# Kernel tuning notes

Hardware: AMD Instinct MI355X
Metric: run time of the kernel (lower is better)

The kernel has to match this reference:

```python
import jax, jax.numpy as jnp
import numpy as np

K = 5        # kernel_size per pseudo-dim
DIM = 2      # pseudo-coordinate dimensionality
K2 = K * K   # total kernel weight matrices
N_NODES = 50000


def spline_basis(edge_attr):
    """Open B-spline basis, degree=1, dim=2. Returns basis [E,4], weight_index [E,4]."""
    v = edge_attr * (K - 1)                      # [E,2], pseudo in [0,1]
    lo = jnp.floor(v)
    frac = v - lo                                # [E,2]
    lo = lo.astype(jnp.int32)
    fac = jnp.stack([1.0 - frac, frac], axis=-1)                 # [E,2,2] (dim, bit)
    idx = jnp.clip(lo[..., None] + jnp.arange(2), 0, K - 1)      # [E,2,2]
    b0 = jnp.array([0, 1, 0, 1])  # bit for dim 0, per spline term
    b1 = jnp.array([0, 0, 1, 1])  # bit for dim 1
    basis = fac[:, 0, b0] * fac[:, 1, b1]        # [E,4]
    wi = idx[:, 0, b0] * K + idx[:, 1, b1]       # [E,4] flat kernel index
    return basis, wi


def spline_conv(x, src, dst, basis, wi, W, root, bias, n_nodes):
    """SplineConv with mean aggregation, root weight and bias.
    x:[N,Fin] W:[K2,Fin,Fout] root:[Fin,Fout] bias:[Fout]"""
    E = src.shape[0]
    K2_, Fin, Fout = W.shape
    # scatter the 4 sparse basis values into a dense per-edge kernel-coeff matrix [E,K2]
    coeff = jnp.zeros((E, K2_), x.dtype).at[jnp.arange(E)[:, None], wi].add(basis)
    xj = x[src]                                  # gather source features [E,Fin]
    msg = jnp.zeros((E, Fout), x.dtype)
    for k in range(K2_):                         # fixed small loop over 25 kernels
        msg = msg + coeff[:, k:k + 1] * (xj @ W[k])
    agg = jax.ops.segment_sum(msg, dst, num_segments=n_nodes)    # [N,Fout]
    deg = jax.ops.segment_sum(jnp.ones((E,), x.dtype), dst, num_segments=n_nodes)
    agg = agg / jnp.clip(deg, 1.0)[:, None]      # mean aggregation
    return agg + x @ root + bias


def setup_inputs() -> dict:
    key = jax.random.key(0)
    ks = jax.random.split(key, 9)
    E = 800000
    Fin, H, C = 64, 16, 7
    x = jax.random.normal(ks[0], (N_NODES, Fin), dtype=jnp.float32)
    edge_index = jax.random.randint(ks[1], (2, E), 0, N_NODES, dtype=jnp.int64)
    edge_attr = jax.random.uniform(ks[2], (E, DIM), dtype=jnp.float32)
    s1 = 1.0 / np.sqrt(Fin)
    s2 = 1.0 / np.sqrt(H)
    W1 = jax.random.uniform(ks[3], (K2, Fin, H), jnp.float32, -s1, s1)
    root1 = jax.random.uniform(ks[4], (Fin, H), jnp.float32, -s1, s1)
    bias1 = jax.random.uniform(ks[5], (H,), jnp.float32, -s1, s1)
    W2 = jax.random.uniform(ks[6], (K2, H, C), jnp.float32, -s2, s2)
    root2 = jax.random.uniform(ks[7], (H, C), jnp.float32, -s2, s2)
    bias2 = jax.random.uniform(ks[8], (C,), jnp.float32, -s2, s2)
    return {"x": x, "edge_index": edge_index, "edge_attr": edge_attr,
            "W1": W1, "root1": root1, "bias1": bias1,
            "W2": W2, "root2": root2, "bias2": bias2}


def reference(x, edge_index, edge_attr, W1, root1, bias1, W2, root2, bias2):
    src = edge_index[0]
    dst = edge_index[1]
    basis, wi = spline_basis(edge_attr)
    h = jax.nn.relu(spline_conv(x, src, dst, basis, wi, W1, root1, bias1, N_NODES))
    # dropout(p=0.6) is identity in eval mode
    out = spline_conv(h, src, dst, basis, wi, W2, root2, bias2, N_NODES)
    return jax.nn.log_softmax(out, axis=1)
```

## Files before the change

kernel.cpp:

```cpp
#include <hip/hip_runtime.h>

#define KK2 25
#define FIN 64
#define HH 16
#define CC 7

#define SCAN_VPT 4
#define SCAN_BLK 256
#define SCAN_CHUNK (SCAN_VPT * SCAN_BLK)

__global__ void k_hist(const int* __restrict__ ei, int* __restrict__ cnt, int E) {
    int e = blockIdx.x * 256 + threadIdx.x;
    if (e < E) atomicAdd(&cnt[ei[E + e]], 1);
}

__global__ void k_bsum(const int* __restrict__ cnt, int* __restrict__ bsum, int N) {
    int b = blockIdx.x, t = threadIdx.x;
    int base = b * SCAN_CHUNK + t * SCAN_VPT;
    int s = 0;
#pragma unroll
    for (int j = 0; j < SCAN_VPT; j++) {
        int i = base + j;
        if (i < N) s += cnt[i];
    }
#pragma unroll
    for (int d = 1; d < 64; d <<= 1) s += __shfl_xor(s, d, 64);
    __shared__ int sd[SCAN_BLK / 64];
    if ((t & 63) == 0) sd[t >> 6] = s;
    __syncthreads();
    if (t == 0) {
        int tot = 0;
        for (int w = 0; w < SCAN_BLK / 64; w++) tot += sd[w];
        bsum[b] = tot;
    }
}

__global__ void k_bscan(const int* __restrict__ bsum, int* __restrict__ boff, int nblk) {
    int t = threadIdx.x;
    __shared__ int sd[256];
    int v = (t < nblk) ? bsum[t] : 0;
    sd[t] = v;
    __syncthreads();
    for (int off = 1; off < 256; off <<= 1) {
        int u = (t >= off) ? sd[t - off] : 0;
        __syncthreads();
        sd[t] += u;
        __syncthreads();
    }
    boff[t] = sd[t] - v;
}

__global__ void k_sfin(const int* __restrict__ cnt, const int* __restrict__ boff,
                       int* __restrict__ rowStart, int* __restrict__ cursor, int N) {
    int b = blockIdx.x, t = threadIdx.x;
    int base = b * SCAN_CHUNK + t * SCAN_VPT;
    int v[SCAN_VPT];
    int s = 0;
#pragma unroll
    for (int j = 0; j < SCAN_VPT; j++) {
        int i = base + j;
        v[j] = (i < N) ? cnt[i] : 0;
        s += v[j];
    }
    __shared__ int sd[SCAN_BLK];
    sd[t] = s;
    __syncthreads();
    for (int off = 1; off < SCAN_BLK; off <<= 1) {
        int u = (t >= off) ? sd[t - off] : 0;
        __syncthreads();
        sd[t] += u;
        __syncthreads();
    }
    int run = sd[t] - s + boff[b];
#pragma unroll
    for (int j = 0; j < SCAN_VPT; j++) {
        int i = base + j;
        if (i < N) {
            rowStart[i] = run;
            cursor[i] = run;
            run += v[j];
            if (i == N - 1) rowStart[N] = run;
        }
    }
}

__global__ void k_scatter(const float* __restrict__ attr, const int* __restrict__ ei,
                          int* __restrict__ cursor, int* __restrict__ eSrc,
                          float4* __restrict__ eBasis, unsigned* __restrict__ eWi, int E) {
    int e = blockIdx.x * 256 + threadIdx.x;
    if (e >= E) return;
    float v0 = attr[2 * e] * 4.0f, v1 = attr[2 * e + 1] * 4.0f;
    float l0 = floorf(v0), l1 = floorf(v1);
    float f0 = v0 - l0, f1 = v1 - l1;
    int i0 = (int)l0, i1 = (int)l1;
    int i0a = min(max(i0, 0), 4), i0b = min(max(i0 + 1, 0), 4);
    int i1a = min(max(i1, 0), 4), i1b = min(max(i1 + 1, 0), 4);
    float4 b;
    b.x = (1.0f - f0) * (1.0f - f1);
    b.y = f0 * (1.0f - f1);
    b.z = (1.0f - f0) * f1;
    b.w = f0 * f1;
    unsigned pack = (unsigned)(i0a * 5 + i1a) | ((unsigned)(i0b * 5 + i1a) << 8) |
                    ((unsigned)(i0a * 5 + i1b) << 16) | ((unsigned)(i0b * 5 + i1b) << 24);
    int s = ei[e], d = ei[E + e];
    int pos = atomicAdd(&cursor[d], 1);
    eSrc[pos] = s;
    eBasis[pos] = b;
    eWi[pos] = pack;
}

__global__ void k_prepW(const float* __restrict__ W1, const float* __restrict__ W2,
                        float* __restrict__ B1t, float* __restrict__ W2p) {
    int tid = blockIdx.x * 256 + threadIdx.x;
    if (tid < KK2 * FIN * HH) {
        int c = tid >> 6, i = tid & 63;
        int k = c >> 4, h = c & 15;
        B1t[tid] = W1[(k * FIN + i) * HH + h];
    }
    if (tid < KK2 * HH * CC) {
        int k = tid / (HH * CC), r = tid % (HH * CC);
        int i = r / CC, c = r % CC;
        W2p[(k * HH + i) * 8 + c] = W2[tid];
    }
}

__global__ void k_y1(const float* __restrict__ x, const float* __restrict__ B1t,
                     float* __restrict__ y1, int N, int nb) {
    int q = blockIdx.x / nb;
    int n = (blockIdx.x % nb) * 256 + threadIdx.x;
    if (n >= N) return;
    float4 xr[16];
    const float4* xp = (const float4*)(x + (size_t)n * 64);
#pragma unroll
    for (int i = 0; i < 16; i++) xr[i] = xp[i];
    const float* B = B1t + q * 100 * 64;
    float4* yo = (float4*)(y1 + (size_t)n * 400 + q * 100);
    for (int cg = 0; cg < 25; cg++) {
        float a0 = 0, a1 = 0, a2 = 0, a3 = 0;
        const float4* b0 = (const float4*)(B + (cg * 4 + 0) * 64);
        const float4* b1 = (const float4*)(B + (cg * 4 + 1) * 64);
        const float4* b2 = (const float4*)(B + (cg * 4 + 2) * 64);
        const float4* b3 = (const float4*)(B + (cg * 4 + 3) * 64);
#pragma unroll
        for (int i = 0; i < 16; i++) {
            float4 xi = xr[i];
            float4 v0 = b0[i], v1 = b1[i], v2 = b2[i], v3 = b3[i];
            a0 += xi.x * v0.x + xi.y * v0.y + xi.z * v0.z + xi.w * v0.w;
            a1 += xi.x * v1.x + xi.y * v1.y + xi.z * v1.z + xi.w * v1.w;
            a2 += xi.x * v2.x + xi.y * v2.y + xi.z * v2.z + xi.w * v2.w;
            a3 += xi.x * v3.x + xi.y * v3.y + xi.z * v3.z + xi.w * v3.w;
        }
        yo[cg] = make_float4(a0, a1, a2, a3);
    }
}

__global__ void k_agg1(const int* __restrict__ rowStart, const int* __restrict__ eSrc,
                       const float4* __restrict__ eBasis, const unsigned* __restrict__ eWi,
                       const float* __restrict__ y1, float* __restrict__ agg1, int N) {
    int n = blockIdx.x * 4 + (threadIdx.x >> 6);
    if (n >= N) return;
    int lane = threadIdx.x & 63;
    int sub = lane >> 4, h = lane & 15;
    int start = rowStart[n], end = rowStart[n + 1];
    float acc = 0.0f;
    for (int i = start + sub; i < end; i += 4) {
        int s = eSrc[i];
        float4 b = eBasis[i];
        unsigned w = eWi[i];
        const float* yr = y1 + (size_t)s * 400;
        acc += b.x * yr[(w & 255u) * 16 + h];
        acc += b.y * yr[((w >> 8) & 255u) * 16 + h];
        acc += b.z * yr[((w >> 16) & 255u) * 16 + h];
        acc += b.w * yr[(w >> 24) * 16 + h];
    }
    acc += __shfl_xor(acc, 16, 64);
    acc += __shfl_xor(acc, 32, 64);
    if (lane < 16) agg1[(size_t)n * 16 + h] = acc;
}

__global__ void k_upd1(const float* __restrict__ x, const float* __restrict__ agg1,
                       const int* __restrict__ rowStart, const float* __restrict__ root1,
                       const float* __restrict__ bias1, float* __restrict__ h1, int N) {
    int n = blockIdx.x * 256 + threadIdx.x;
    if (n >= N) return;
    float inv = 1.0f / (float)max(rowStart[n + 1] - rowStart[n], 1);
    float r[16];
#pragma unroll
    for (int h = 0; h < 16; h++) r[h] = agg1[(size_t)n * 16 + h] * inv + bias1[h];
    const float* xrow = x + (size_t)n * 64;
    for (int i = 0; i < 64; i++) {
        float xi = xrow[i];
        const float* rr = root1 + i * 16;
#pragma unroll
        for (int h = 0; h < 16; h++) r[h] += xi * rr[h];
    }
    float* ho = h1 + (size_t)n * 16;
#pragma unroll
    for (int h = 0; h < 16; h++) ho[h] = fmaxf(r[h], 0.0f);
}

__global__ void k_y2(const float* __restrict__ h1, const float* __restrict__ W2p,
                     float* __restrict__ y2, int N) {
    int n = blockIdx.x * 256 + threadIdx.x;
    if (n >= N) return;
    float h[16];
    const float4* hp = (const float4*)(h1 + (size_t)n * 16);
#pragma unroll
    for (int j = 0; j < 4; j++) {
        float4 v = hp[j];
        h[4 * j] = v.x; h[4 * j + 1] = v.y; h[4 * j + 2] = v.z; h[4 * j + 3] = v.w;
    }
    float4* yo = (float4*)(y2 + (size_t)n * 200);
    for (int k = 0; k < 25; k++) {
        float4 zlo = make_float4(0, 0, 0, 0), zhi = make_float4(0, 0, 0, 0);
        const float4* wp = (const float4*)(W2p + k * 128);
#pragma unroll
        for (int i = 0; i < 16; i++) {
            float hi = h[i];
            float4 lo = wp[2 * i], hv = wp[2 * i + 1];
            zlo.x += hi * lo.x; zlo.y += hi * lo.y; zlo.z += hi * lo.z; zlo.w += hi * lo.w;
            zhi.x += hi * hv.x; zhi.y += hi * hv.y; zhi.z += hi * hv.z; zhi.w += hi * hv.w;
        }
        yo[2 * k] = zlo;
        yo[2 * k + 1] = zhi;
    }
}

__global__ void k_agg2(const int* __restrict__ rowStart, const int* __restrict__ eSrc,
                       const float4* __restrict__ eBasis, const unsigned* __restrict__ eWi,
                       const float* __restrict__ y2, float* __restrict__ agg2, int N) {
    int n = blockIdx.x * 4 + (threadIdx.x >> 6);
    if (n >= N) return;
    int lane = threadIdx.x & 63;
    int sub = lane >> 3, c = lane & 7;
    int start = rowStart[n], end = rowStart[n + 1];
    float acc = 0.0f;
    for (int i = start + sub; i < end; i += 8) {
        int s = eSrc[i];
        float4 b = eBasis[i];
        unsigned w = eWi[i];
        const float* yr = y2 + (size_t)s * 200;
        acc += b.x * yr[(w & 255u) * 8 + c];
        acc += b.y * yr[((w >> 8) & 255u) * 8 + c];
        acc += b.z * yr[((w >> 16) & 255u) * 8 + c];
        acc += b.w * yr[(w >> 24) * 8 + c];
    }
    acc += __shfl_xor(acc, 8, 64);
    acc += __shfl_xor(acc, 16, 64);
    acc += __shfl_xor(acc, 32, 64);
    if (lane < 8) agg2[(size_t)n * 8 + c] = acc;
}

__global__ void k_fin2(const float* __restrict__ h1, const float* __restrict__ agg2,
                       const int* __restrict__ rowStart, const float* __restrict__ root2,
                       const float* __restrict__ bias2, float* __restrict__ out, int N) {
    int n = blockIdx.x * 256 + threadIdx.x;
    if (n >= N) return;
    float inv = 1.0f / (float)max(rowStart[n + 1] - rowStart[n], 1);
    float z[7];
#pragma unroll
    for (int c = 0; c < 7; c++) z[c] = agg2[(size_t)n * 8 + c] * inv + bias2[c];
    const float* hrow = h1 + (size_t)n * 16;
#pragma unroll
    for (int i = 0; i < 16; i++) {
        float hi = hrow[i];
        const float* rr = root2 + i * 7;
#pragma unroll
        for (int c = 0; c < 7; c++) z[c] += hi * rr[c];
    }
    float m = z[0];
#pragma unroll
    for (int c = 1; c < 7; c++) m = fmaxf(m, z[c]);
    float ssum = 0.0f;
#pragma unroll
    for (int c = 0; c < 7; c++) ssum += expf(z[c] - m);
    float ls = logf(ssum);
    float* orow = out + (size_t)n * 7;
#pragma unroll
    for (int c = 0; c < 7; c++) orow[c] = z[c] - m - ls;
}

extern "C" void kernel_launch(void* const* d_in, const int* in_sizes, int n_in,
                              void* d_out, int out_size, void* d_ws, size_t ws_size,
                              hipStream_t stream) {
    const float* x     = (const float*)d_in[0];
    const int*   ei    = (const int*)d_in[1];
    const float* attr  = (const float*)d_in[2];
    const float* W1    = (const float*)d_in[3];
    const float* root1 = (const float*)d_in[4];
    const float* bias1 = (const float*)d_in[5];
    const float* W2    = (const float*)d_in[6];
    const float* root2 = (const float*)d_in[7];
    const float* bias2 = (const float*)d_in[8];
    float* out = (float*)d_out;

    int N = in_sizes[0] / FIN;
    int E = in_sizes[1] / 2;

    char* w = (char*)d_ws;
    size_t off = 0;
    auto alloc = [&](size_t bytes) -> void* {
        void* p = w + off;
        off += (bytes + 255) & ~(size_t)255;
        return p;
    };
    int*      cnt      = (int*)alloc((size_t)N * 4);
    int*      rowStart = (int*)alloc((size_t)(N + 1) * 4);
    int*      cursor   = (int*)alloc((size_t)N * 4);
    int*      bsum     = (int*)alloc(260 * 4);
    int*      boff     = (int*)alloc(260 * 4);
    int*      eSrc     = (int*)alloc((size_t)E * 4);
    float4*   eBasis   = (float4*)alloc((size_t)E * 16);
    unsigned* eWi      = (unsigned*)alloc((size_t)E * 4);
    float*    agg1     = (float*)alloc((size_t)N * 64);
    float*    h1       = (float*)alloc((size_t)N * 64);
    float*    agg2     = (float*)alloc((size_t)N * 32);
    float*    B1t      = (float*)alloc((size_t)KK2 * FIN * HH * 4);
    float*    W2p      = (float*)alloc((size_t)KK2 * HH * 8 * 4);
    float*    y1       = (float*)alloc((size_t)N * 400 * 4);
    float*    y2       = y1;
    (void)ws_size; (void)n_in; (void)out_size;

    hipMemsetAsync(cnt, 0, (size_t)N * 4, stream);

    int ebl = (E + 255) / 256;
    int nbl = (N + 255) / 256;
    int sblk = (N + SCAN_CHUNK - 1) / SCAN_CHUNK;

    k_hist<<<ebl, 256, 0, stream>>>(ei, cnt, E);
    k_bsum<<<sblk, SCAN_BLK, 0, stream>>>(cnt, bsum, N);
    k_bscan<<<1, 256, 0, stream>>>(bsum, boff, sblk);
    k_sfin<<<sblk, SCAN_BLK, 0, stream>>>(cnt, boff, rowStart, cursor, N);
    k_scatter<<<ebl, 256, 0, stream>>>(attr, ei, cursor, eSrc, eBasis, eWi, E);
    k_prepW<<<(KK2 * FIN * HH + 255) / 256, 256, 0, stream>>>(W1, W2, B1t, W2p);
    k_y1<<<4 * nbl, 256, 0, stream>>>(x, B1t, y1, N, nbl);
    k_agg1<<<(N + 3) / 4, 256, 0, stream>>>(rowStart, eSrc, eBasis, eWi, y1, agg1, N);
    k_upd1<<<nbl, 256, 0, stream>>>(x, agg1, rowStart, root1, bias1, h1, N);
    k_y2<<<nbl, 256, 0, stream>>>(h1, W2p, y2, N);
    k_agg2<<<(N + 3) / 4, 256, 0, stream>>>(rowStart, eSrc, eBasis, eWi, y2, agg2, N);
    k_fin2<<<nbl, 256, 0, stream>>>(h1, agg2, rowStart, root2, bias2, out, N);
}
```

Measured before the change: 323.7 us.

## Pack edge records into 32-byte structs and split y1 precompute into five groups

The three per-edge arrays (source, basis, packed weight indices) are merged into one 32-byte record of two float4s, so each edge in the aggregation kernels is read with two vector loads from one cache line instead of three separate streams. Record size grows from 24 to 32 bytes, adding write and read traffic. k_y1 now uses five groups of 80 outputs instead of four of 100, holding the results in registers and storing them at the end of the loop. That gives more blocks but raises register pressure.

```diff
diff --git a/kernel.cpp b/kernel.cpp
--- a/kernel.cpp
+++ b/kernel.cpp
@@ -85,8 +85,7 @@
 }
 
 __global__ void k_scatter(const float* __restrict__ attr, const int* __restrict__ ei,
-                          int* __restrict__ cursor, int* __restrict__ eSrc,
-                          float4* __restrict__ eBasis, unsigned* __restrict__ eWi, int E) {
+                          int* __restrict__ cursor, float4* __restrict__ rec, int E) {
     int e = blockIdx.x * 256 + threadIdx.x;
     if (e >= E) return;
     float v0 = attr[2 * e] * 4.0f, v1 = attr[2 * e + 1] * 4.0f;
@@ -104,9 +103,8 @@
                     ((unsigned)(i0a * 5 + i1b) << 16) | ((unsigned)(i0b * 5 + i1b) << 24);
     int s = ei[e], d = ei[E + e];
     int pos = atomicAdd(&cursor[d], 1);
-    eSrc[pos] = s;
-    eBasis[pos] = b;
-    eWi[pos] = pack;
+    rec[2 * pos] = b;
+    rec[2 * pos + 1] = make_float4(__int_as_float(s), __uint_as_float(pack), 0.0f, 0.0f);
 }
 
 __global__ void k_prepW(const float* __restrict__ W1, const float* __restrict__ W2,
@@ -126,16 +124,17 @@
 
 __global__ void k_y1(const float* __restrict__ x, const float* __restrict__ B1t,
                      float* __restrict__ y1, int N, int nb) {
-    int q = blockIdx.x / nb;
+    int g = blockIdx.x / nb;
     int n = (blockIdx.x % nb) * 256 + threadIdx.x;
     if (n >= N) return;
     float4 xr[16];
     const float4* xp = (const float4*)(x + (size_t)n * 64);
 #pragma unroll
     for (int i = 0; i < 16; i++) xr[i] = xp[i];
-    const float* B = B1t + q * 100 * 64;
-    float4* yo = (float4*)(y1 + (size_t)n * 400 + q * 100);
-    for (int cg = 0; cg < 25; cg++) {
+    const float* B = B1t + g * 80 * 64;
+    float4 acc[20];
+#pragma unroll
+    for (int cg = 0; cg < 20; cg++) {
         float a0 = 0, a1 = 0, a2 = 0, a3 = 0;
         const float4* b0 = (const float4*)(B + (cg * 4 + 0) * 64);
         const float4* b1 = (const float4*)(B + (cg * 4 + 1) * 64);
@@ -150,12 +149,14 @@
             a2 += xi.x * v2.x + xi.y * v2.y + xi.z * v2.z + xi.w * v2.w;
             a3 += xi.x * v3.x + xi.y * v3.y + xi.z * v3.z + xi.w * v3.w;
         }
-        yo[cg] = make_float4(a0, a1, a2, a3);
-    }
-}
-
-__global__ void k_agg1(const int* __restrict__ rowStart, const int* __restrict__ eSrc,
-                       const float4* __restrict__ eBasis, const unsigned* __restrict__ eWi,
+        acc[cg] = make_float4(a0, a1, a2, a3);
+    }
+    float4* yo = (float4*)(y1 + (size_t)n * 400 + g * 80);
+#pragma unroll
+    for (int cg = 0; cg < 20; cg++) yo[cg] = acc[cg];
+}
+
+__global__ void k_agg1(const int* __restrict__ rowStart, const float4* __restrict__ rec,
                        const float* __restrict__ y1, float* __restrict__ agg1, int N) {
     int n = blockIdx.x * 4 + (threadIdx.x >> 6);
     if (n >= N) return;
@@ -164,9 +165,10 @@
     int start = rowStart[n], end = rowStart[n + 1];
     float acc = 0.0f;
     for (int i = start + sub; i < end; i += 4) {
-        int s = eSrc[i];
-        float4 b = eBasis[i];
-        unsigned w = eWi[i];
+        float4 b = rec[2 * i];
+        float4 meta = rec[2 * i + 1];
+        int s = __float_as_int(meta.x);
+        unsigned w = __float_as_uint(meta.y);
         const float* yr = y1 + (size_t)s * 400;
         acc += b.x * yr[(w & 255u) * 16 + h];
         acc += b.y * yr[((w >> 8) & 255u) * 16 + h];
@@ -226,8 +228,7 @@
     }
 }
 
-__global__ void k_agg2(const int* __restrict__ rowStart, const int* __restrict__ eSrc,
-                       const float4* __restrict__ eBasis, const unsigned* __restrict__ eWi,
+__global__ void k_agg2(const int* __restrict__ rowStart, const float4* __restrict__ rec,
                        const float* __restrict__ y2, float* __restrict__ agg2, int N) {
     int n = blockIdx.x * 4 + (threadIdx.x >> 6);
     if (n >= N) return;
@@ -236,9 +237,10 @@
     int start = rowStart[n], end = rowStart[n + 1];
     float acc = 0.0f;
     for (int i = start + sub; i < end; i += 8) {
-        int s = eSrc[i];
-        float4 b = eBasis[i];
-        unsigned w = eWi[i];
+        float4 b = rec[2 * i];
+        float4 meta = rec[2 * i + 1];
+        int s = __float_as_int(meta.x);
+        unsigned w = __float_as_uint(meta.y);
         const float* yr = y2 + (size_t)s * 200;
         acc += b.x * yr[(w & 255u) * 8 + c];
         acc += b.y * yr[((w >> 8) & 255u) * 8 + c];
@@ -309,9 +311,7 @@
     int*      cursor   = (int*)alloc((size_t)N * 4);
     int*      bsum     = (int*)alloc(260 * 4);
     int*      boff     = (int*)alloc(260 * 4);
-    int*      eSrc     = (int*)alloc((size_t)E * 4);
-    float4*   eBasis   = (float4*)alloc((size_t)E * 16);
-    unsigned* eWi      = (unsigned*)alloc((size_t)E * 4);
+    float4*   rec      = (float4*)alloc((size_t)E * 32);
     float*    agg1     = (float*)alloc((size_t)N * 64);
     float*    h1       = (float*)alloc((size_t)N * 64);
     float*    agg2     = (float*)alloc((size_t)N * 32);
@@ -331,12 +331,12 @@
     k_bsum<<<sblk, SCAN_BLK, 0, stream>>>(cnt, bsum, N);
     k_bscan<<<1, 256, 0, stream>>>(bsum, boff, sblk);
     k_sfin<<<sblk, SCAN_BLK, 0, stream>>>(cnt, boff, rowStart, cursor, N);
-    k_scatter<<<ebl, 256, 0, stream>>>(attr, ei, cursor, eSrc, eBasis, eWi, E);
+    k_scatter<<<ebl, 256, 0, stream>>>(attr, ei, cursor, rec, E);
     k_prepW<<<(KK2 * FIN * HH + 255) / 256, 256, 0, stream>>>(W1, W2, B1t, W2p);
-    k_y1<<<4 * nbl, 256, 0, stream>>>(x, B1t, y1, N, nbl);
-    k_agg1<<<(N + 3) / 4, 256, 0, stream>>>(rowStart, eSrc, eBasis, eWi, y1, agg1, N);
+    k_y1<<<5 * nbl, 256, 0, stream>>>(x, B1t, y1, N, nbl);
+    k_agg1<<<(N + 3) / 4, 256, 0, stream>>>(rowStart, rec, y1, agg1, N);
     k_upd1<<<nbl, 256, 0, stream>>>(x, agg1, rowStart, root1, bias1, h1, N);
     k_y2<<<nbl, 256, 0, stream>>>(h1, W2p, y2, N);
-    k_agg2<<<(N + 3) / 4, 256, 0, stream>>>(rowStart, eSrc, eBasis, eWi, y2, agg2, N);
+    k_agg2<<<(N + 3) / 4, 256, 0, stream>>>(rowStart, rec, y2, agg2, N);
     k_fin2<<<nbl, 256, 0, stream>>>(h1, agg2, rowStart, root2, bias2, out, N);
 }
```

Measured after the change: 343.8 us. +6.2%, slower.
